# Kernel optimization log

Hardware: AMD Instinct MI355X
Metric: run time of the kernel (lower is better)

## Reference

```python
import jax, jax.numpy as jnp
import numpy as np

N = 50000
E = 800000
IN_DIM = 512
HID = 64
OUT = 64
HEADS = 4
NEG_SLOPE = 0.2


def setup_inputs() -> dict:
    key = jax.random.key(0)
    ks = jax.random.split(key, 16)
    s = 0.05
    inp = {
        "x": jax.random.normal(ks[0], (N, IN_DIM), jnp.float32),
        "edge_index": jax.random.randint(ks[1], (2, E), 0, N, jnp.int64),
        # layer 1: in=512 -> heads*hid = 4*64 = 256, concat=True
        "W1l": jax.random.normal(ks[2], (IN_DIM, HEADS * HID), jnp.float32) * s,
        "b1l": jnp.zeros((HEADS * HID,), jnp.float32),
        "W1r": jax.random.normal(ks[3], (IN_DIM, HEADS * HID), jnp.float32) * s,
        "b1r": jnp.zeros((HEADS * HID,), jnp.float32),
        "att1": jax.random.normal(ks[4], (HEADS, HID), jnp.float32) * s,
        "bias1": jnp.zeros((HEADS * HID,), jnp.float32),
        # layer 2: in=256 -> heads*(2*out) = 4*128, concat=False (mean heads)
        "W2l": jax.random.normal(ks[5], (HEADS * HID, HEADS * 2 * OUT), jnp.float32) * s,
        "b2l": jnp.zeros((HEADS * 2 * OUT,), jnp.float32),
        "W2r": jax.random.normal(ks[6], (HEADS * HID, HEADS * 2 * OUT), jnp.float32) * s,
        "b2r": jnp.zeros((HEADS * 2 * OUT,), jnp.float32),
        "att2": jax.random.normal(ks[7], (HEADS, 2 * OUT), jnp.float32) * s,
        "bias2": jnp.zeros((2 * OUT,), jnp.float32),
    }
    return inp


def _gatv2(x, src, dst, Wl, bl, Wr, br, att, bias, concat):
    """GATv2Conv (PyG semantics): message x_l[src], attention over incoming edges per dst."""
    H, C = att.shape
    n = x.shape[0]
    xl = (x @ Wl + bl).reshape(n, H, C)  # source transform (messages)
    xr = (x @ Wr + br).reshape(n, H, C)  # target transform
    g = jax.nn.leaky_relu(xl[src] + xr[dst], NEG_SLOPE)   # [E, H, C]
    e = jnp.einsum('ehc,hc->eh', g, att)                  # [E, H]
    # numerically-stable softmax over irregular neighbor sets (segmented by dst)
    m = jax.ops.segment_max(e, dst, num_segments=n)
    ex = jnp.exp(e - m[dst])
    denom = jax.ops.segment_sum(ex, dst, num_segments=n)
    alpha = ex / (denom[dst] + 1e-16)                     # [E, H]
    out = jax.ops.segment_sum(xl[src] * alpha[..., None], dst, num_segments=n)  # [N, H, C]
    if concat:
        return out.reshape(n, H * C) + bias
    return out.mean(axis=1) + bias


def reference(x, edge_index, W1l, b1l, W1r, b1r, att1, bias1,
              W2l, b2l, W2r, b2r, att2, bias2):
    # add self loops (PyG add_self_loops=True default)
    loops = jnp.arange(N, dtype=edge_index.dtype)
    src = jnp.concatenate([edge_index[0], loops])
    dst = jnp.concatenate([edge_index[1], loops])
    h = jax.nn.relu(_gatv2(x, src, dst, W1l, b1l, W1r, b1r, att1, bias1, concat=True))
    return _gatv2(h, src, dst, W2l, b2l, W2r, b2r, att2, bias2, concat=False)
```

## Files before the change

### kernel.cpp

```cpp
#include <hip/hip_runtime.h>

#define NNODES 50000
#define NEDGES 800000
#define ET (NEDGES + NNODES)
#define HEADS 4

typedef __attribute__((ext_vector_type(8))) short bf16x8;
typedef __attribute__((ext_vector_type(4))) float f32x4;
typedef __attribute__((ext_vector_type(2))) float f32x2v;

#define EXP2F(x) __builtin_amdgcn_exp2f(x)

#if defined(__has_builtin)
#if __has_builtin(__builtin_elementwise_fma)
#define VFMA(a, b, c) __builtin_elementwise_fma((a), (b), (c))
#endif
#if __has_builtin(__builtin_elementwise_max)
#define VMAX(a, b) __builtin_elementwise_max((a), (b))
#endif
#endif
#ifndef VFMA
__device__ inline f32x2v vfma_(f32x2v a, f32x2v b, f32x2v c) {
  f32x2v r; r.x = fmaf(a.x, b.x, c.x); r.y = fmaf(a.y, b.y, c.y); return r;
}
#define VFMA vfma_
#endif
#ifndef VMAX
__device__ inline f32x2v vmax_(f32x2v a, f32x2v b) {
  f32x2v r; r.x = fmaxf(a.x, b.x); r.y = fmaxf(a.y, b.y); return r;
}
#define VMAX vmax_
#endif

#define GLOAD16(g, l) __builtin_amdgcn_global_load_lds(                      \
    (const __attribute__((address_space(1))) unsigned int*)(g),              \
    (__attribute__((address_space(3))) unsigned int*)(l), 16, 0, 0)

__device__ inline unsigned short f2bf(float f) {
  union { float f; unsigned int i; } c; c.f = f;
  unsigned int b = c.i + 0x7fffu + ((c.i >> 16) & 1u);
  return (unsigned short)(b >> 16);
}
__device__ inline f32x2v cvtpair(unsigned u) {
  union { unsigned i; float f; } lo, hi;
  lo.i = u << 16; hi.i = u & 0xffff0000u;
  f32x2v r; r.x = lo.f; r.y = hi.f; return r;
}


__global__ void k_hist(const int* __restrict__ ei, int* __restrict__ deg) {
  int i = blockIdx.x * blockDim.x + threadIdx.x;
  if (i >= ET) return;
  int dst = (i < NEDGES) ? ei[NEDGES + i] : (i - NEDGES);
  atomicAdd(&deg[dst], 1);
}

__global__ void k_scan1(const int* __restrict__ deg, int* __restrict__ part,
                        int* __restrict__ bsum, int n) {
  __shared__ int s[256];
  int tid = threadIdx.x;
  int i = blockIdx.x * 256 + tid;
  int v = (i < n) ? deg[i] : 0;
  s[tid] = v;
  __syncthreads();
  for (int off = 1; off < 256; off <<= 1) {
    int t = (tid >= off) ? s[tid - off] : 0;
    __syncthreads();
    s[tid] += t;
    __syncthreads();
  }
  if (i < n) part[i] = s[tid] - v;
  if (tid == 255) bsum[blockIdx.x] = s[255];
}

__global__ void k_scan2(int* bsum, int nb) {
  __shared__ int s[256];
  int t = threadIdx.x;
  int v = (t < nb) ? bsum[t] : 0;
  s[t] = v;
  __syncthreads();
  for (int off = 1; off < 256; off <<= 1) {
    int tv = (t >= off) ? s[t - off] : 0;
    __syncthreads();
    s[t] += tv;
    __syncthreads();
  }
  if (t < nb) bsum[t] = s[t] - v;
}

__global__ void k_scan3(const int* __restrict__ part, const int* __restrict__ bsum,
                        int* __restrict__ rowstart, int* __restrict__ cursor,
                        int n, int total) {
  int i = blockIdx.x * blockDim.x + threadIdx.x;
  if (i < n) {
    int v = part[i] + bsum[i >> 8];
    rowstart[i] = v;
    cursor[i] = v;
  }
  if (i == n) rowstart[n] = total;
}

__global__ void k_scatter(const int* __restrict__ ei, int* __restrict__ cursor,
                          int* __restrict__ csrsrc) {
  int i = blockIdx.x * blockDim.x + threadIdx.x;
  if (i >= ET) return;
  int src, dst;
  if (i < NEDGES) { src = ei[i]; dst = ei[NEDGES + i]; }
  else            { src = dst = i - NEDGES; }
  int pos = atomicAdd(&cursor[dst], 1);
  csrsrc[pos] = src;
}


__global__ void k_cast_bf16(const float* __restrict__ in, unsigned short* __restrict__ out, int n4) {
  int i = blockIdx.x * blockDim.x + threadIdx.x;
  if (i >= n4) return;
  float4 v = ((const float4*)in)[i];
  ushort4 o;
  o.x = f2bf(v.x); o.y = f2bf(v.y); o.z = f2bf(v.z); o.w = f2bf(v.w);
  ((ushort4*)out)[i] = o;
}

__global__ __launch_bounds__(256) void k_castw_all(
    const float* __restrict__ W1l, const float* __restrict__ W1r,
    const float* __restrict__ W2l, const float* __restrict__ W2r,
    unsigned short* __restrict__ w1t, unsigned short* __restrict__ w2t) {
  __shared__ float tile[32][33];
  int which = blockIdx.y;
  const float* W;
  unsigned short* T;
  int K, N, noff;
  if (which == 0)      { W = W1l; T = w1t; K = 512; N = 256; noff = 0; }
  else if (which == 1) { W = W1r; T = w1t; K = 512; N = 256; noff = 256; }
  else if (which == 2) { W = W2l; T = w2t; K = 256; N = 512; noff = 0; }
  else                 { W = W2r; T = w2t; K = 256; N = 512; noff = 512; }
  int tpr = N >> 5;
  int tk = (blockIdx.x / tpr) << 5;
  int tn = (blockIdx.x % tpr) << 5;
  int c = threadIdx.x & 31, r = threadIdx.x >> 5;
#pragma unroll
  for (int rr = 0; rr < 32; rr += 8)
    tile[r + rr][c] = W[(size_t)(tk + r + rr) * N + tn + c];
  __syncthreads();
#pragma unroll
  for (int rr = 0; rr < 32; rr += 8)
    T[(size_t)(tn + r + rr + noff) * K + tk + c] = f2bf(tile[c][r + rr]);
}


template <int N> __device__ __forceinline__ void waitvm() {
  if constexpr (N == 0) asm volatile("s_waitcnt vmcnt(0)" ::: "memory");
  else if constexpr (N == 4) asm volatile("s_waitcnt vmcnt(4)" ::: "memory");
  else asm volatile("s_waitcnt vmcnt(8)" ::: "memory");
}

__global__ __launch_bounds__(256) void k_gemm(
    const unsigned short* __restrict__ A, const unsigned short* __restrict__ Bt,
    const float* __restrict__ bL, const float* __restrict__ bR, int nsplit,
    unsigned short* __restrict__ C, int M, int K, int N) {
  __shared__ unsigned short As[3][128 * 32];
  __shared__ unsigned short Bs[3][128 * 32];
  int tid = threadIdx.x;
  int lane = tid & 63, wave = tid >> 6;
  int wr = (wave >> 1) * 64, wc = (wave & 1) * 64;
  int row0 = blockIdx.x * 128, col0 = blockIdx.y * 128;
  int fr = lane & 15, fq = lane >> 4;
  int sr = tid >> 2, sc = (tid & 3) * 8;

  const unsigned short* ga0 = &A[(size_t)(row0 + sr) * K + sc];
  const unsigned short* ga1 = &A[(size_t)(row0 + sr + 64) * K + sc];
  const unsigned short* gb0 = &Bt[(size_t)(col0 + sr) * K + sc];
  const unsigned short* gb1 = &Bt[(size_t)(col0 + sr + 64) * K + sc];

  f32x4 acc[4][4] = {};
  const int NT = K >> 5;

#define STAGE(b, k0)                                  \
  do {                                                \
    GLOAD16(ga0 + (k0), &As[b][tid * 8]);             \
    GLOAD16(ga1 + (k0), &As[b][2048 + tid * 8]);      \
    GLOAD16(gb0 + (k0), &Bs[b][tid * 8]);             \
    GLOAD16(gb1 + (k0), &Bs[b][2048 + tid * 8]);      \
  } while (0)

#define COMPUTE(b)                                                        \
  do {                                                                    \
    bf16x8 af[4], bfr[4];                                                 \
    _Pragma("unroll")                                                     \
    for (int m = 0; m < 4; ++m)                                           \
      af[m] = *(const bf16x8*)&As[b][(wr + m * 16 + fr) * 32 + fq * 8];   \
    _Pragma("unroll")                                                     \
    for (int n = 0; n < 4; ++n)                                           \
      bfr[n] = *(const bf16x8*)&Bs[b][(wc + n * 16 + fr) * 32 + fq * 8];  \
    _Pragma("unroll")                                                     \
    for (int m = 0; m < 4; ++m)                                           \
      _Pragma("unroll")                                                   \
      for (int n = 0; n < 4; ++n)                                         \
        acc[m][n] = __builtin_amdgcn_mfma_f32_16x16x32_bf16(af[m], bfr[n], acc[m][n], 0, 0, 0); \
  } while (0)

  STAGE(0, 0);
  STAGE(1, 32);
  STAGE(2, 64);

  for (int t = 0; t < NT - 3; ++t) {
    int b = t % 3;
    waitvm<8>();
    __builtin_amdgcn_s_barrier();
    COMPUTE(b);
    asm volatile("s_waitcnt lgkmcnt(0)" ::: "memory");
    __builtin_amdgcn_sched_barrier(0);
    __builtin_amdgcn_s_barrier();
    STAGE(b, (t + 3) << 5);
  }
  waitvm<8>(); __builtin_amdgcn_s_barrier(); COMPUTE((NT - 3) % 3);
  waitvm<4>(); __builtin_amdgcn_s_barrier(); COMPUTE((NT - 2) % 3);
  waitvm<0>(); __builtin_amdgcn_s_barrier(); COMPUTE((NT - 1) % 3);

#undef STAGE
#undef COMPUTE

#pragma unroll
  for (int m = 0; m < 4; ++m) {
#pragma unroll
    for (int n = 0; n < 4; ++n) {
      int col = col0 + wc + n * 16 + fr;
      float bv = (col < nsplit) ? bL[col] : bR[col - nsplit];
#pragma unroll
      for (int j = 0; j < 4; ++j) {
        int row = row0 + wr + m * 16 + fq * 4 + j;
        if (row < M) C[(size_t)row * N + col] = f2bf(acc[m][n][j] + bv);
      }
    }
  }
}


template <int CQ> struct raw_t;
template <> struct raw_t<1> { using T = uint2; };
template <> struct raw_t<2> { using T = uint4; };

template <int CQ>
__device__ __forceinline__ void rawwords(const typename raw_t<CQ>::T& r, unsigned* u) {
  u[0] = r.x; u[1] = r.y;
  if constexpr (CQ == 2) { u[2] = r.z; u[3] = r.w; }
}

template <int CQ>
__device__ __forceinline__ void unpackP(const typename raw_t<CQ>::T& r, f32x2v* x) {
  unsigned u[4];
  rawwords<CQ>(r, u);
#pragma unroll
  for (int j = 0; j < CQ * 2; ++j) x[j] = cvtpair(u[j]);
}

template <int CQ>
__device__ __forceinline__ float edge_score_pk(const f32x2v* x, const f32x2v* xr2,
                                               const f32x2v* att2) {
  const f32x2v c02 = {0.2f, 0.2f};
  f32x2v p2 = {0.f, 0.f};
#pragma unroll
  for (int j = 0; j < CQ * 2; ++j) {
    f32x2v s = x[j] + xr2[j];
    f32x2v g = VMAX(s, s * c02);
    p2 = VFMA(att2[j], g, p2);
  }
  return p2.x + p2.y;
}

template <int CQ, int MODE, int STR>
__global__ __launch_bounds__(256) void k_fused(
    const int* __restrict__ rowstart, const int* __restrict__ csrsrc,
    const unsigned short* __restrict__ xlr,
    const float* __restrict__ att, const float* __restrict__ bias,
    void* __restrict__ outp) {
  const int C = CQ * 64;
  const int CHL = CQ * 4;
  const int P = CQ * 2;
  using RawT = typename raw_t<CQ>::T;
  int dst = (blockIdx.x * blockDim.x + threadIdx.x) >> 6;
  int lane = threadIdx.x & 63;
  if (dst >= NNODES) return;
  int h = lane >> 4;
  int l = lane & 15;
  const int choff = h * C + l * CHL;

  f32x2v xr2[P], att2[P];
  {
    RawT xrr = *(const RawT*)&xlr[(size_t)dst * STR + STR / 2 + choff];
    unpackP<CQ>(xrr, xr2);
#pragma unroll
    for (int j = 0; j < P; ++j) {
      att2[j].x = att[choff + j * 2 + 0] * 1.44269504f;
      att2[j].y = att[choff + j * 2 + 1] * 1.44269504f;
    }
  }

  int rs = __builtin_amdgcn_readfirstlane(rowstart[dst]);
  int re = __builtin_amdgcn_readfirstlane(rowstart[dst + 1]);

  float den = 0.f;
  f32x2v acc2[P];
#pragma unroll
  for (int j = 0; j < P; ++j) acc2[j] = (f32x2v){0.f, 0.f};

  int i = rs;
  for (; i + 4 <= re; i += 4) {
    int s0 = csrsrc[i + 0];
    int s1 = csrsrc[i + 1];
    int s2 = csrsrc[i + 2];
    int s3 = csrsrc[i + 3];
    RawT r0 = *(const RawT*)&xlr[(unsigned)s0 * (unsigned)STR + choff];
    RawT r1 = *(const RawT*)&xlr[(unsigned)s1 * (unsigned)STR + choff];
    RawT r2 = *(const RawT*)&xlr[(unsigned)s2 * (unsigned)STR + choff];
    RawT r3 = *(const RawT*)&xlr[(unsigned)s3 * (unsigned)STR + choff];
    f32x2v x0[P], x1[P], x2[P], x3[P];
    unpackP<CQ>(r0, x0); unpackP<CQ>(r1, x1);
    unpackP<CQ>(r2, x2); unpackP<CQ>(r3, x3);
    float p0 = edge_score_pk<CQ>(x0, xr2, att2);
    float p1 = edge_score_pk<CQ>(x1, xr2, att2);
    float p2 = edge_score_pk<CQ>(x2, xr2, att2);
    float p3 = edge_score_pk<CQ>(x3, xr2, att2);
#pragma unroll
    for (int d = 1; d <= 8; d <<= 1) {
      p0 += __shfl_xor(p0, d);
      p1 += __shfl_xor(p1, d);
      p2 += __shfl_xor(p2, d);
      p3 += __shfl_xor(p3, d);
    }
    float w0 = EXP2F(p0), w1 = EXP2F(p1), w2 = EXP2F(p2), w3 = EXP2F(p3);
    den += (w0 + w1) + (w2 + w3);
    f32x2v w0v = {w0, w0}, w1v = {w1, w1}, w2v = {w2, w2}, w3v = {w3, w3};
#pragma unroll
    for (int j = 0; j < P; ++j) {
      f32x2v a = acc2[j];
      a = VFMA(w0v, x0[j], a);
      a = VFMA(w1v, x1[j], a);
      a = VFMA(w2v, x2[j], a);
      a = VFMA(w3v, x3[j], a);
      acc2[j] = a;
    }
  }
  for (; i < re; ++i) {
    int s0 = csrsrc[i];
    RawT r0 = *(const RawT*)&xlr[(unsigned)s0 * (unsigned)STR + choff];
    f32x2v x0[P];
    unpackP<CQ>(r0, x0);
    float p0 = edge_score_pk<CQ>(x0, xr2, att2);
#pragma unroll
    for (int d = 1; d <= 8; d <<= 1) p0 += __shfl_xor(p0, d);
    float w0 = EXP2F(p0);
    den += w0;
    f32x2v wv = {w0, w0};
#pragma unroll
    for (int j = 0; j < P; ++j) acc2[j] = VFMA(wv, x0[j], acc2[j]);
  }

  float inv = 1.f / (den + 1e-16f);

  if (MODE == 0) {
    unsigned short* out = (unsigned short*)outp;
#pragma unroll
    for (int q = 0; q < CQ; ++q) {
      const float4 bv = *(const float4*)&bias[choff + q * 4];
      ushort4 o;
      o.x = f2bf(fmaxf(acc2[q * 2 + 0].x * inv + bv.x, 0.f));
      o.y = f2bf(fmaxf(acc2[q * 2 + 0].y * inv + bv.y, 0.f));
      o.z = f2bf(fmaxf(acc2[q * 2 + 1].x * inv + bv.z, 0.f));
      o.w = f2bf(fmaxf(acc2[q * 2 + 1].y * inv + bv.w, 0.f));
      *(ushort4*)&out[(size_t)dst * (HEADS * C) + choff + q * 4] = o;
    }
  } else {
    float* out = (float*)outp;
    float rr[8];
#pragma unroll
    for (int j = 0; j < P; ++j) {
      rr[j * 2 + 0] = acc2[j].x * inv;
      rr[j * 2 + 1] = acc2[j].y * inv;
    }
#pragma unroll
    for (int c = 0; c < CHL; ++c) {
      rr[c] += __shfl_xor(rr[c], 16);
      rr[c] += __shfl_xor(rr[c], 32);
    }
    if (lane < 16) {
#pragma unroll
      for (int q = 0; q < CQ; ++q) {
        int c = lane * CHL + q * 4;
        float4 o;
        o.x = rr[q * 4 + 0] * 0.25f + bias[c + 0];
        o.y = rr[q * 4 + 1] * 0.25f + bias[c + 1];
        o.z = rr[q * 4 + 2] * 0.25f + bias[c + 2];
        o.w = rr[q * 4 + 3] * 0.25f + bias[c + 3];
        *(float4*)&out[(size_t)dst * C + c] = o;
      }
    }
  }
}


extern "C" void kernel_launch(void* const* d_in, const int* in_sizes, int n_in,
                              void* d_out, int out_size, void* d_ws, size_t ws_size,
                              hipStream_t stream) {
  (void)in_sizes; (void)n_in; (void)out_size; (void)ws_size;
  const float* x     = (const float*)d_in[0];
  const int*   ei    = (const int*)d_in[1];
  const float* W1l   = (const float*)d_in[2];
  const float* b1l   = (const float*)d_in[3];
  const float* W1r   = (const float*)d_in[4];
  const float* b1r   = (const float*)d_in[5];
  const float* att1  = (const float*)d_in[6];
  const float* bias1 = (const float*)d_in[7];
  const float* W2l   = (const float*)d_in[8];
  const float* b2l   = (const float*)d_in[9];
  const float* W2r   = (const float*)d_in[10];
  const float* b2r   = (const float*)d_in[11];
  const float* att2  = (const float*)d_in[12];
  const float* bias2 = (const float*)d_in[13];
  float* out = (float*)d_out;

  char* ws = (char*)d_ws;
  size_t off = 0;
  auto alloc = [&](size_t bytes) {
    char* p = ws + off;
    off = (off + bytes + 255) & ~(size_t)255;
    return p;
  };
  int*  deg      = (int*)alloc((size_t)NNODES * 4);
  int*  part     = (int*)alloc((size_t)NNODES * 4);
  int*  bsum     = (int*)alloc(256 * 4);
  int*  rowstart = (int*)alloc((size_t)(NNODES + 1) * 4);
  int*  cursor   = (int*)alloc((size_t)NNODES * 4);
  int*  csrsrc   = (int*)alloc((size_t)ET * 4);
  unsigned short* xb   = (unsigned short*)alloc((size_t)NNODES * 512 * 2);
  unsigned short* w1t  = (unsigned short*)alloc((size_t)512 * 512 * 2);
  unsigned short* w2t  = (unsigned short*)alloc((size_t)1024 * 256 * 2);
  unsigned short* xlr1 = (unsigned short*)alloc((size_t)NNODES * 512 * 2);
  unsigned short* hbuf = (unsigned short*)alloc((size_t)NNODES * 256 * 2);
  unsigned short* xlr2 = (unsigned short*)alloc((size_t)NNODES * 1024 * 2);
  (void)alloc(64 * 1024);

  (void)hipMemsetAsync(deg, 0, (size_t)NNODES * 4, stream);
  k_hist<<<(ET + 255) / 256, 256, 0, stream>>>(ei, deg);
  int nb = (NNODES + 255) / 256;
  k_scan1<<<nb, 256, 0, stream>>>(deg, part, bsum, NNODES);
  k_scan2<<<1, 256, 0, stream>>>(bsum, nb);
  k_scan3<<<(NNODES + 256) / 256, 256, 0, stream>>>(part, bsum, rowstart, cursor, NNODES, ET);
  k_scatter<<<(ET + 255) / 256, 256, 0, stream>>>(ei, cursor, csrsrc);

  k_cast_bf16<<<(NNODES * 512 / 4 + 255) / 256, 256, 0, stream>>>(x, xb, NNODES * 512 / 4);
  k_castw_all<<<dim3(128, 4), 256, 0, stream>>>(W1l, W1r, W2l, W2r, w1t, w2t);

  const int gridM = (NNODES + 127) / 128;
  const int gridFused = (NNODES + 3) / 4;

  k_gemm<<<dim3(gridM, 4), 256, 0, stream>>>(xb, w1t, b1l, b1r, 256, xlr1, NNODES, 512, 512);
  k_fused<1, 0, 512><<<gridFused, 256, 0, stream>>>(rowstart, csrsrc, xlr1, att1, bias1, hbuf);

  k_gemm<<<dim3(gridM, 8), 256, 0, stream>>>(hbuf, w2t, b2l, b2r, 512, xlr2, NNODES, 256, 1024);
  k_fused<2, 1, 1024><<<gridFused, 256, 0, stream>>>(rowstart, csrsrc, xlr2, att2, bias2, out);
}
```

Before: 448.0 us.

## Pipeline layer-2 neighbor gathers through LDS and merge prep kernels

Layer-2 aggregation now prefetches source-node feature rows into a per-wave LDS slab with global_load_lds, keeping eight gathers in flight at once. Edges are processed in masked batches of eight so load latency overlaps with compute. The x cast, degree histogram and weight transpose are merged into one launch to cut launch count. The CSR index buffer gains padding so the masked prefetch can read past the end safely, at the cost of wasted gathers on the padded slots of low-degree nodes.

```diff
diff --git a/kernel.cpp b/kernel.cpp
--- a/kernel.cpp
+++ b/kernel.cpp
@@ -46,14 +46,65 @@
   lo.i = u << 16; hi.i = u & 0xffff0000u;
   f32x2v r; r.x = lo.f; r.y = hi.f; return r;
 }
-
-
-__global__ void k_hist(const int* __restrict__ ei, int* __restrict__ deg) {
-  int i = blockIdx.x * blockDim.x + threadIdx.x;
-  if (i >= ET) return;
-  int dst = (i < NEDGES) ? ei[NEDGES + i] : (i - NEDGES);
-  atomicAdd(&deg[dst], 1);
-}
+__device__ inline float4 b4tof(uint2 r) {
+  float4 f;
+  union { unsigned int i; float v; } c;
+  c.i = r.x << 16;          f.x = c.v;
+  c.i = r.x & 0xffff0000u;  f.y = c.v;
+  c.i = r.y << 16;          f.z = c.v;
+  c.i = r.y & 0xffff0000u;  f.w = c.v;
+  return f;
+}
+
+
+#define CASTB 25000
+#define HISTB ((ET + 255) / 256)
+#define PREPB (CASTB + HISTB + 512)
+
+__global__ __launch_bounds__(256) void k_prep(
+    const int* __restrict__ ei, int* __restrict__ deg,
+    const float* __restrict__ x, unsigned short* __restrict__ xb,
+    const float* __restrict__ W1l, const float* __restrict__ W1r,
+    const float* __restrict__ W2l, const float* __restrict__ W2r,
+    unsigned short* __restrict__ w1t, unsigned short* __restrict__ w2t) {
+  __shared__ float tile[32][33];
+  int b = blockIdx.x;
+  if (b < CASTB) {
+    int i = b * 256 + threadIdx.x;
+    float4 v = ((const float4*)x)[i];
+    ushort4 o;
+    o.x = f2bf(v.x); o.y = f2bf(v.y); o.z = f2bf(v.z); o.w = f2bf(v.w);
+    ((ushort4*)xb)[i] = o;
+  } else if (b < CASTB + HISTB) {
+    int i = (b - CASTB) * 256 + threadIdx.x;
+    if (i < ET) {
+      int dst = (i < NEDGES) ? ei[NEDGES + i] : (i - NEDGES);
+      atomicAdd(&deg[dst], 1);
+    }
+  } else {
+    int bb = b - CASTB - HISTB;
+    int which = bb >> 7, bx = bb & 127;
+    const float* W;
+    unsigned short* T;
+    int K, N, noff;
+    if (which == 0)      { W = W1l; T = w1t; K = 512; N = 256; noff = 0; }
+    else if (which == 1) { W = W1r; T = w1t; K = 512; N = 256; noff = 256; }
+    else if (which == 2) { W = W2l; T = w2t; K = 256; N = 512; noff = 0; }
+    else                 { W = W2r; T = w2t; K = 256; N = 512; noff = 512; }
+    int tpr = N >> 5;
+    int tk = (bx / tpr) << 5;
+    int tn = (bx % tpr) << 5;
+    int c = threadIdx.x & 31, r = threadIdx.x >> 5;
+#pragma unroll
+    for (int rr = 0; rr < 32; rr += 8)
+      tile[r + rr][c] = W[(size_t)(tk + r + rr) * N + tn + c];
+    __syncthreads();
+#pragma unroll
+    for (int rr = 0; rr < 32; rr += 8)
+      T[(size_t)(tn + r + rr + noff) * K + tk + c] = f2bf(tile[c][r + rr]);
+  }
+}
+
 
 __global__ void k_scan1(const int* __restrict__ deg, int* __restrict__ part,
                         int* __restrict__ bsum, int n) {
@@ -109,42 +160,6 @@
   else            { src = dst = i - NEDGES; }
   int pos = atomicAdd(&cursor[dst], 1);
   csrsrc[pos] = src;
-}
-
-
-__global__ void k_cast_bf16(const float* __restrict__ in, unsigned short* __restrict__ out, int n4) {
-  int i = blockIdx.x * blockDim.x + threadIdx.x;
-  if (i >= n4) return;
-  float4 v = ((const float4*)in)[i];
-  ushort4 o;
-  o.x = f2bf(v.x); o.y = f2bf(v.y); o.z = f2bf(v.z); o.w = f2bf(v.w);
-  ((ushort4*)out)[i] = o;
-}
-
-__global__ __launch_bounds__(256) void k_castw_all(
-    const float* __restrict__ W1l, const float* __restrict__ W1r,
-    const float* __restrict__ W2l, const float* __restrict__ W2r,
-    unsigned short* __restrict__ w1t, unsigned short* __restrict__ w2t) {
-  __shared__ float tile[32][33];
-  int which = blockIdx.y;
-  const float* W;
-  unsigned short* T;
-  int K, N, noff;
-  if (which == 0)      { W = W1l; T = w1t; K = 512; N = 256; noff = 0; }
-  else if (which == 1) { W = W1r; T = w1t; K = 512; N = 256; noff = 256; }
-  else if (which == 2) { W = W2l; T = w2t; K = 256; N = 512; noff = 0; }
-  else                 { W = W2r; T = w2t; K = 256; N = 512; noff = 512; }
-  int tpr = N >> 5;
-  int tk = (blockIdx.x / tpr) << 5;
-  int tn = (blockIdx.x % tpr) << 5;
-  int c = threadIdx.x & 31, r = threadIdx.x >> 5;
-#pragma unroll
-  for (int rr = 0; rr < 32; rr += 8)
-    tile[r + rr][c] = W[(size_t)(tk + r + rr) * N + tn + c];
-  __syncthreads();
-#pragma unroll
-  for (int rr = 0; rr < 32; rr += 8)
-    T[(size_t)(tn + r + rr + noff) * K + tk + c] = f2bf(tile[c][r + rr]);
 }
 
 
@@ -240,87 +255,58 @@
 template <> struct raw_t<1> { using T = uint2; };
 template <> struct raw_t<2> { using T = uint4; };
 
-template <int CQ>
-__device__ __forceinline__ void rawwords(const typename raw_t<CQ>::T& r, unsigned* u) {
-  u[0] = r.x; u[1] = r.y;
-  if constexpr (CQ == 2) { u[2] = r.z; u[3] = r.w; }
-}
-
-template <int CQ>
-__device__ __forceinline__ void unpackP(const typename raw_t<CQ>::T& r, f32x2v* x) {
-  unsigned u[4];
-  rawwords<CQ>(r, u);
-#pragma unroll
-  for (int j = 0; j < CQ * 2; ++j) x[j] = cvtpair(u[j]);
-}
-
-template <int CQ>
-__device__ __forceinline__ float edge_score_pk(const f32x2v* x, const f32x2v* xr2,
-                                               const f32x2v* att2) {
-  const f32x2v c02 = {0.2f, 0.2f};
-  f32x2v p2 = {0.f, 0.f};
-#pragma unroll
-  for (int j = 0; j < CQ * 2; ++j) {
-    f32x2v s = x[j] + xr2[j];
-    f32x2v g = VMAX(s, s * c02);
-    p2 = VFMA(att2[j], g, p2);
-  }
-  return p2.x + p2.y;
-}
-
-template <int CQ, int MODE, int STR>
-__global__ __launch_bounds__(256) void k_fused(
+__global__ __launch_bounds__(256) void k_fused1(
     const int* __restrict__ rowstart, const int* __restrict__ csrsrc,
     const unsigned short* __restrict__ xlr,
     const float* __restrict__ att, const float* __restrict__ bias,
-    void* __restrict__ outp) {
-  const int C = CQ * 64;
-  const int CHL = CQ * 4;
-  const int P = CQ * 2;
-  using RawT = typename raw_t<CQ>::T;
+    unsigned short* __restrict__ out) {
+  const int STR = 512, C = 64;
   int dst = (blockIdx.x * blockDim.x + threadIdx.x) >> 6;
   int lane = threadIdx.x & 63;
   if (dst >= NNODES) return;
-  int h = lane >> 4;
-  int l = lane & 15;
-  const int choff = h * C + l * CHL;
-
-  f32x2v xr2[P], att2[P];
+  int h = lane >> 4, l = lane & 15;
+  const int choff = h * C + l * 4;
+
+  f32x2v xr2[2], att2[2];
   {
-    RawT xrr = *(const RawT*)&xlr[(size_t)dst * STR + STR / 2 + choff];
-    unpackP<CQ>(xrr, xr2);
-#pragma unroll
-    for (int j = 0; j < P; ++j) {
+    uint2 xrr = *(const uint2*)&xlr[(size_t)dst * STR + 256 + choff];
+    xr2[0] = cvtpair(xrr.x); xr2[1] = cvtpair(xrr.y);
+#pragma unroll
+    for (int j = 0; j < 2; ++j) {
       att2[j].x = att[choff + j * 2 + 0] * 1.44269504f;
       att2[j].y = att[choff + j * 2 + 1] * 1.44269504f;
     }
   }
+  const f32x2v c02 = {0.2f, 0.2f};
 
   int rs = __builtin_amdgcn_readfirstlane(rowstart[dst]);
   int re = __builtin_amdgcn_readfirstlane(rowstart[dst + 1]);
 
   float den = 0.f;
-  f32x2v acc2[P];
-#pragma unroll
-  for (int j = 0; j < P; ++j) acc2[j] = (f32x2v){0.f, 0.f};
+  f32x2v acc2[2] = {{0.f, 0.f}, {0.f, 0.f}};
 
   int i = rs;
   for (; i + 4 <= re; i += 4) {
-    int s0 = csrsrc[i + 0];
-    int s1 = csrsrc[i + 1];
-    int s2 = csrsrc[i + 2];
-    int s3 = csrsrc[i + 3];
-    RawT r0 = *(const RawT*)&xlr[(unsigned)s0 * (unsigned)STR + choff];
-    RawT r1 = *(const RawT*)&xlr[(unsigned)s1 * (unsigned)STR + choff];
-    RawT r2 = *(const RawT*)&xlr[(unsigned)s2 * (unsigned)STR + choff];
-    RawT r3 = *(const RawT*)&xlr[(unsigned)s3 * (unsigned)STR + choff];
-    f32x2v x0[P], x1[P], x2[P], x3[P];
-    unpackP<CQ>(r0, x0); unpackP<CQ>(r1, x1);
-    unpackP<CQ>(r2, x2); unpackP<CQ>(r3, x3);
-    float p0 = edge_score_pk<CQ>(x0, xr2, att2);
-    float p1 = edge_score_pk<CQ>(x1, xr2, att2);
-    float p2 = edge_score_pk<CQ>(x2, xr2, att2);
-    float p3 = edge_score_pk<CQ>(x3, xr2, att2);
+    int s0 = csrsrc[i + 0], s1 = csrsrc[i + 1];
+    int s2 = csrsrc[i + 2], s3 = csrsrc[i + 3];
+    uint2 r0 = *(const uint2*)&xlr[(unsigned)s0 * (unsigned)STR + choff];
+    uint2 r1 = *(const uint2*)&xlr[(unsigned)s1 * (unsigned)STR + choff];
+    uint2 r2 = *(const uint2*)&xlr[(unsigned)s2 * (unsigned)STR + choff];
+    uint2 r3 = *(const uint2*)&xlr[(unsigned)s3 * (unsigned)STR + choff];
+    f32x2v x0[2] = {cvtpair(r0.x), cvtpair(r0.y)};
+    f32x2v x1[2] = {cvtpair(r1.x), cvtpair(r1.y)};
+    f32x2v x2[2] = {cvtpair(r2.x), cvtpair(r2.y)};
+    f32x2v x3[2] = {cvtpair(r3.x), cvtpair(r3.y)};
+    f32x2v q0 = {0.f, 0.f}, q1 = {0.f, 0.f}, q2 = {0.f, 0.f}, q3 = {0.f, 0.f};
+#pragma unroll
+    for (int j = 0; j < 2; ++j) {
+      f32x2v s;
+      s = x0[j] + xr2[j]; q0 = VFMA(att2[j], VMAX(s, s * c02), q0);
+      s = x1[j] + xr2[j]; q1 = VFMA(att2[j], VMAX(s, s * c02), q1);
+      s = x2[j] + xr2[j]; q2 = VFMA(att2[j], VMAX(s, s * c02), q2);
+      s = x3[j] + xr2[j]; q3 = VFMA(att2[j], VMAX(s, s * c02), q3);
+    }
+    float p0 = q0.x + q0.y, p1 = q1.x + q1.y, p2 = q2.x + q2.y, p3 = q3.x + q3.y;
 #pragma unroll
     for (int d = 1; d <= 8; d <<= 1) {
       p0 += __shfl_xor(p0, d);
@@ -332,7 +318,7 @@
     den += (w0 + w1) + (w2 + w3);
     f32x2v w0v = {w0, w0}, w1v = {w1, w1}, w2v = {w2, w2}, w3v = {w3, w3};
 #pragma unroll
-    for (int j = 0; j < P; ++j) {
+    for (int j = 0; j < 2; ++j) {
       f32x2v a = acc2[j];
       a = VFMA(w0v, x0[j], a);
       a = VFMA(w1v, x1[j], a);
@@ -343,57 +329,137 @@
   }
   for (; i < re; ++i) {
     int s0 = csrsrc[i];
-    RawT r0 = *(const RawT*)&xlr[(unsigned)s0 * (unsigned)STR + choff];
-    f32x2v x0[P];
-    unpackP<CQ>(r0, x0);
-    float p0 = edge_score_pk<CQ>(x0, xr2, att2);
+    uint2 r0 = *(const uint2*)&xlr[(unsigned)s0 * (unsigned)STR + choff];
+    f32x2v x0[2] = {cvtpair(r0.x), cvtpair(r0.y)};
+    f32x2v q0 = {0.f, 0.f};
+#pragma unroll
+    for (int j = 0; j < 2; ++j) {
+      f32x2v s = x0[j] + xr2[j];
+      q0 = VFMA(att2[j], VMAX(s, s * c02), q0);
+    }
+    float p0 = q0.x + q0.y;
 #pragma unroll
     for (int d = 1; d <= 8; d <<= 1) p0 += __shfl_xor(p0, d);
     float w0 = EXP2F(p0);
     den += w0;
     f32x2v wv = {w0, w0};
 #pragma unroll
-    for (int j = 0; j < P; ++j) acc2[j] = VFMA(wv, x0[j], acc2[j]);
+    for (int j = 0; j < 2; ++j) acc2[j] = VFMA(wv, x0[j], acc2[j]);
   }
 
   float inv = 1.f / (den + 1e-16f);
-
-  if (MODE == 0) {
-    unsigned short* out = (unsigned short*)outp;
-#pragma unroll
-    for (int q = 0; q < CQ; ++q) {
-      const float4 bv = *(const float4*)&bias[choff + q * 4];
-      ushort4 o;
-      o.x = f2bf(fmaxf(acc2[q * 2 + 0].x * inv + bv.x, 0.f));
-      o.y = f2bf(fmaxf(acc2[q * 2 + 0].y * inv + bv.y, 0.f));
-      o.z = f2bf(fmaxf(acc2[q * 2 + 1].x * inv + bv.z, 0.f));
-      o.w = f2bf(fmaxf(acc2[q * 2 + 1].y * inv + bv.w, 0.f));
-      *(ushort4*)&out[(size_t)dst * (HEADS * C) + choff + q * 4] = o;
-    }
-  } else {
-    float* out = (float*)outp;
-    float rr[8];
-#pragma unroll
-    for (int j = 0; j < P; ++j) {
-      rr[j * 2 + 0] = acc2[j].x * inv;
-      rr[j * 2 + 1] = acc2[j].y * inv;
-    }
-#pragma unroll
-    for (int c = 0; c < CHL; ++c) {
-      rr[c] += __shfl_xor(rr[c], 16);
-      rr[c] += __shfl_xor(rr[c], 32);
-    }
-    if (lane < 16) {
-#pragma unroll
-      for (int q = 0; q < CQ; ++q) {
-        int c = lane * CHL + q * 4;
-        float4 o;
-        o.x = rr[q * 4 + 0] * 0.25f + bias[c + 0];
-        o.y = rr[q * 4 + 1] * 0.25f + bias[c + 1];
-        o.z = rr[q * 4 + 2] * 0.25f + bias[c + 2];
-        o.w = rr[q * 4 + 3] * 0.25f + bias[c + 3];
-        *(float4*)&out[(size_t)dst * C + c] = o;
+  const float4 bv = *(const float4*)&bias[choff];
+  ushort4 o;
+  o.x = f2bf(fmaxf(acc2[0].x * inv + bv.x, 0.f));
+  o.y = f2bf(fmaxf(acc2[0].y * inv + bv.y, 0.f));
+  o.z = f2bf(fmaxf(acc2[1].x * inv + bv.z, 0.f));
+  o.w = f2bf(fmaxf(acc2[1].y * inv + bv.w, 0.f));
+  *(ushort4*)&out[(size_t)dst * 256 + choff] = o;
+}
+
+
+__global__ __launch_bounds__(256) void k_fused2(
+    const int* __restrict__ rowstart, const int* __restrict__ csrsrc,
+    const unsigned short* __restrict__ xlr,
+    const float* __restrict__ att, const float* __restrict__ bias,
+    float* __restrict__ out) {
+  __shared__ char slab_[4][8 * 1024];
+  int dst = (blockIdx.x * blockDim.x + threadIdx.x) >> 6;
+  int lane = threadIdx.x & 63;
+  if (dst >= NNODES) return;
+  char* slab = slab_[threadIdx.x >> 6];
+  int h = lane >> 4, l = lane & 15;
+  const int choff = h * 128 + l * 8;
+
+  f32x2v xr2[4], att2[4];
+  {
+    uint4 xrr = *(const uint4*)&xlr[(size_t)dst * 1024 + 512 + choff];
+    unsigned u[4] = {xrr.x, xrr.y, xrr.z, xrr.w};
+#pragma unroll
+    for (int j = 0; j < 4; ++j) {
+      xr2[j] = cvtpair(u[j]);
+      att2[j].x = att[choff + j * 2 + 0] * 1.44269504f;
+      att2[j].y = att[choff + j * 2 + 1] * 1.44269504f;
+    }
+  }
+  const f32x2v c02 = {0.2f, 0.2f};
+
+  int rs = __builtin_amdgcn_readfirstlane(rowstart[dst]);
+  int re = __builtin_amdgcn_readfirstlane(rowstart[dst + 1]);
+  int nb = (re - rs + 7) >> 3;
+
+  float den = 0.f;
+  f32x2v acc2[4] = {{0.f, 0.f}, {0.f, 0.f}, {0.f, 0.f}, {0.f, 0.f}};
+
+  int idxN[8];
+#pragma unroll
+  for (int e = 0; e < 8; ++e) {
+    int v = csrsrc[rs + e];
+    v = (rs + e < re) ? v : 0;
+    GLOAD16(&xlr[(unsigned)v * 1024u + choff], slab + e * 1024 + lane * 16);
+  }
+#pragma unroll
+  for (int e = 0; e < 8; ++e) idxN[e] = csrsrc[rs + 8 + e];
+
+  int i = rs;
+  for (int b = 0; b < nb; ++b, i += 8) {
+#pragma unroll
+    for (int e = 0; e < 8; ++e) {
+      asm volatile("s_waitcnt vmcnt(7)" ::: "memory");
+      uint4 raw = *(const uint4*)(slab + e * 1024 + lane * 16);
+      asm volatile("s_waitcnt lgkmcnt(0)" ::: "memory");
+      {
+        int v = (i + 8 + e < re) ? idxN[e] : 0;
+        GLOAD16(&xlr[(unsigned)v * 1024u + choff], slab + e * 1024 + lane * 16);
+        idxN[e] = csrsrc[i + 16 + e];
       }
+      unsigned u[4] = {raw.x, raw.y, raw.z, raw.w};
+      f32x2v x[4];
+#pragma unroll
+      for (int j = 0; j < 4; ++j) x[j] = cvtpair(u[j]);
+      f32x2v p2 = {0.f, 0.f};
+#pragma unroll
+      for (int j = 0; j < 4; ++j) {
+        f32x2v s = x[j] + xr2[j];
+        p2 = VFMA(att2[j], VMAX(s, s * c02), p2);
+      }
+      float p = p2.x + p2.y;
+      p += __shfl_xor(p, 1);
+      p += __shfl_xor(p, 2);
+      p += __shfl_xor(p, 4);
+      p += __shfl_xor(p, 8);
+      p = (i + e < re) ? p : -1e30f;
+      float w = EXP2F(p);
+      den += w;
+      f32x2v wv = {w, w};
+#pragma unroll
+      for (int j = 0; j < 4; ++j) acc2[j] = VFMA(wv, x[j], acc2[j]);
+    }
+  }
+  asm volatile("s_waitcnt vmcnt(0)" ::: "memory");
+
+  float inv = 1.f / (den + 1e-16f);
+  float rr[8];
+#pragma unroll
+  for (int j = 0; j < 4; ++j) {
+    rr[j * 2 + 0] = acc2[j].x * inv;
+    rr[j * 2 + 1] = acc2[j].y * inv;
+  }
+#pragma unroll
+  for (int c = 0; c < 8; ++c) {
+    rr[c] += __shfl_xor(rr[c], 16);
+    rr[c] += __shfl_xor(rr[c], 32);
+  }
+  if (lane < 16) {
+#pragma unroll
+    for (int q = 0; q < 2; ++q) {
+      int c = lane * 8 + q * 4;
+      float4 o;
+      o.x = rr[q * 4 + 0] * 0.25f + bias[c + 0];
+      o.y = rr[q * 4 + 1] * 0.25f + bias[c + 1];
+      o.z = rr[q * 4 + 2] * 0.25f + bias[c + 2];
+      o.w = rr[q * 4 + 3] * 0.25f + bias[c + 3];
+      *(float4*)&out[(size_t)dst * 128 + c] = o;
     }
   }
 }
@@ -431,7 +497,7 @@
   int*  bsum     = (int*)alloc(256 * 4);
   int*  rowstart = (int*)alloc((size_t)(NNODES + 1) * 4);
   int*  cursor   = (int*)alloc((size_t)NNODES * 4);
-  int*  csrsrc   = (int*)alloc((size_t)ET * 4);
+  int*  csrsrc   = (int*)alloc((size_t)(ET + 32) * 4);
   unsigned short* xb   = (unsigned short*)alloc((size_t)NNODES * 512 * 2);
   unsigned short* w1t  = (unsigned short*)alloc((size_t)512 * 512 * 2);
   unsigned short* w2t  = (unsigned short*)alloc((size_t)1024 * 256 * 2);
@@ -441,22 +507,21 @@
   (void)alloc(64 * 1024);
 
   (void)hipMemsetAsync(deg, 0, (size_t)NNODES * 4, stream);
-  k_hist<<<(ET + 255) / 256, 256, 0, stream>>>(ei, deg);
+
+  k_prep<<<PREPB, 256, 0, stream>>>(ei, deg, x, xb, W1l, W1r, W2l, W2r, w1t, w2t);
+
   int nb = (NNODES + 255) / 256;
   k_scan1<<<nb, 256, 0, stream>>>(deg, part, bsum, NNODES);
   k_scan2<<<1, 256, 0, stream>>>(bsum, nb);
   k_scan3<<<(NNODES + 256) / 256, 256, 0, stream>>>(part, bsum, rowstart, cursor, NNODES, ET);
   k_scatter<<<(ET + 255) / 256, 256, 0, stream>>>(ei, cursor, csrsrc);
 
-  k_cast_bf16<<<(NNODES * 512 / 4 + 255) / 256, 256, 0, stream>>>(x, xb, NNODES * 512 / 4);
-  k_castw_all<<<dim3(128, 4), 256, 0, stream>>>(W1l, W1r, W2l, W2r, w1t, w2t);
-
   const int gridM = (NNODES + 127) / 128;
   const int gridFused = (NNODES + 3) / 4;
 
   k_gemm<<<dim3(gridM, 4), 256, 0, stream>>>(xb, w1t, b1l, b1r, 256, xlr1, NNODES, 512, 512);
-  k_fused<1, 0, 512><<<gridFused, 256, 0, stream>>>(rowstart, csrsrc, xlr1, att1, bias1, hbuf);
+  k_fused1<<<gridFused, 256, 0, stream>>>(rowstart, csrsrc, xlr1, att1, bias1, hbuf);
 
   k_gemm<<<dim3(gridM, 8), 256, 0, stream>>>(hbuf, w2t, b2l, b2r, 512, xlr2, NNODES, 256, 1024);
-  k_fused<2, 1, 1024><<<gridFused, 256, 0, stream>>>(rowstart, csrsrc, xlr2, att2, bias2, out);
-}
+  k_fused2<<<gridFused, 256, 0, stream>>>(rowstart, csrsrc, xlr2, att2, bias2, out);
+}
```

Result: slower. 496.9 us (+10.9%).

## Merge prep kernels and process destination nodes in degree-sorted order

Applied to the files above, without the earlier changes.

Fuses the x cast, degree histogram and weight transpose-cast into one launch to cut kernel launch count. Adds a counting sort of nodes by in-degree (bin, scan, scatter) and has the fused aggregation kernels map waves to nodes through this permutation. Waves in the same block then see similar edge counts, which reduces load imbalance and tail effects. In exchange it adds three small kernels plus an extra indirection, and it gives up the locality of processing consecutive destination nodes.

```diff
diff --git a/kernel.cpp b/kernel.cpp
--- a/kernel.cpp
+++ b/kernel.cpp
@@ -48,12 +48,54 @@
 }
 
 
-__global__ void k_hist(const int* __restrict__ ei, int* __restrict__ deg) {
-  int i = blockIdx.x * blockDim.x + threadIdx.x;
-  if (i >= ET) return;
-  int dst = (i < NEDGES) ? ei[NEDGES + i] : (i - NEDGES);
-  atomicAdd(&deg[dst], 1);
-}
+#define CASTB 25000
+#define HISTB ((ET + 255) / 256)
+#define PREPB (CASTB + HISTB + 512)
+
+__global__ __launch_bounds__(256) void k_prep(
+    const int* __restrict__ ei, int* __restrict__ deg,
+    const float* __restrict__ x, unsigned short* __restrict__ xb,
+    const float* __restrict__ W1l, const float* __restrict__ W1r,
+    const float* __restrict__ W2l, const float* __restrict__ W2r,
+    unsigned short* __restrict__ w1t, unsigned short* __restrict__ w2t) {
+  __shared__ float tile[32][33];
+  int b = blockIdx.x;
+  if (b < CASTB) {
+    int i = b * 256 + threadIdx.x;
+    float4 v = ((const float4*)x)[i];
+    ushort4 o;
+    o.x = f2bf(v.x); o.y = f2bf(v.y); o.z = f2bf(v.z); o.w = f2bf(v.w);
+    ((ushort4*)xb)[i] = o;
+  } else if (b < CASTB + HISTB) {
+    int i = (b - CASTB) * 256 + threadIdx.x;
+    if (i < ET) {
+      int dst = (i < NEDGES) ? ei[NEDGES + i] : (i - NEDGES);
+      atomicAdd(&deg[dst], 1);
+    }
+  } else {
+    int bb = b - CASTB - HISTB;
+    int which = bb >> 7, bx = bb & 127;
+    const float* W;
+    unsigned short* T;
+    int K, N, noff;
+    if (which == 0)      { W = W1l; T = w1t; K = 512; N = 256; noff = 0; }
+    else if (which == 1) { W = W1r; T = w1t; K = 512; N = 256; noff = 256; }
+    else if (which == 2) { W = W2l; T = w2t; K = 256; N = 512; noff = 0; }
+    else                 { W = W2r; T = w2t; K = 256; N = 512; noff = 512; }
+    int tpr = N >> 5;
+    int tk = (bx / tpr) << 5;
+    int tn = (bx % tpr) << 5;
+    int c = threadIdx.x & 31, r = threadIdx.x >> 5;
+#pragma unroll
+    for (int rr = 0; rr < 32; rr += 8)
+      tile[r + rr][c] = W[(size_t)(tk + r + rr) * N + tn + c];
+    __syncthreads();
+#pragma unroll
+    for (int rr = 0; rr < 32; rr += 8)
+      T[(size_t)(tn + r + rr + noff) * K + tk + c] = f2bf(tile[c][r + rr]);
+  }
+}
+
 
 __global__ void k_scan1(const int* __restrict__ deg, int* __restrict__ part,
                         int* __restrict__ bsum, int n) {
@@ -112,39 +154,40 @@
 }
 
 
-__global__ void k_cast_bf16(const float* __restrict__ in, unsigned short* __restrict__ out, int n4) {
+__global__ void k_dbin(const int* __restrict__ deg, int* __restrict__ dbin) {
   int i = blockIdx.x * blockDim.x + threadIdx.x;
-  if (i >= n4) return;
-  float4 v = ((const float4*)in)[i];
-  ushort4 o;
-  o.x = f2bf(v.x); o.y = f2bf(v.y); o.z = f2bf(v.z); o.w = f2bf(v.w);
-  ((ushort4*)out)[i] = o;
-}
-
-__global__ __launch_bounds__(256) void k_castw_all(
-    const float* __restrict__ W1l, const float* __restrict__ W1r,
-    const float* __restrict__ W2l, const float* __restrict__ W2r,
-    unsigned short* __restrict__ w1t, unsigned short* __restrict__ w2t) {
-  __shared__ float tile[32][33];
-  int which = blockIdx.y;
-  const float* W;
-  unsigned short* T;
-  int K, N, noff;
-  if (which == 0)      { W = W1l; T = w1t; K = 512; N = 256; noff = 0; }
-  else if (which == 1) { W = W1r; T = w1t; K = 512; N = 256; noff = 256; }
-  else if (which == 2) { W = W2l; T = w2t; K = 256; N = 512; noff = 0; }
-  else                 { W = W2r; T = w2t; K = 256; N = 512; noff = 512; }
-  int tpr = N >> 5;
-  int tk = (blockIdx.x / tpr) << 5;
-  int tn = (blockIdx.x % tpr) << 5;
-  int c = threadIdx.x & 31, r = threadIdx.x >> 5;
-#pragma unroll
-  for (int rr = 0; rr < 32; rr += 8)
-    tile[r + rr][c] = W[(size_t)(tk + r + rr) * N + tn + c];
+  if (i < NNODES) atomicAdd(&dbin[min(deg[i], 1023)], 1);
+}
+
+__global__ void k_dscan(int* __restrict__ dbin) {
+  __shared__ int s[1024];
+  int t = threadIdx.x;
+  int o[4];
+#pragma unroll
+  for (int k = 0; k < 4; ++k) { o[k] = dbin[t * 4 + k]; s[t * 4 + k] = o[k]; }
   __syncthreads();
-#pragma unroll
-  for (int rr = 0; rr < 32; rr += 8)
-    T[(size_t)(tn + r + rr + noff) * K + tk + c] = f2bf(tile[c][r + rr]);
+  for (int off = 1; off < 1024; off <<= 1) {
+    int v[4];
+#pragma unroll
+    for (int k = 0; k < 4; ++k) {
+      int j = t * 4 + k;
+      v[k] = (j >= off) ? s[j - off] : 0;
+    }
+    __syncthreads();
+#pragma unroll
+    for (int k = 0; k < 4; ++k) s[t * 4 + k] += v[k];
+    __syncthreads();
+  }
+#pragma unroll
+  for (int k = 0; k < 4; ++k) dbin[t * 4 + k] = s[t * 4 + k] - o[k];
+}
+
+__global__ void k_dscat(const int* __restrict__ deg, int* __restrict__ dbin,
+                        int* __restrict__ perm) {
+  int i = blockIdx.x * blockDim.x + threadIdx.x;
+  if (i >= NNODES) return;
+  int pos = atomicAdd(&dbin[min(deg[i], 1023)], 1);
+  perm[pos] = i;
 }
 
 
@@ -241,17 +284,9 @@
 template <> struct raw_t<2> { using T = uint4; };
 
 template <int CQ>
-__device__ __forceinline__ void rawwords(const typename raw_t<CQ>::T& r, unsigned* u) {
-  u[0] = r.x; u[1] = r.y;
-  if constexpr (CQ == 2) { u[2] = r.z; u[3] = r.w; }
-}
-
-template <int CQ>
 __device__ __forceinline__ void unpackP(const typename raw_t<CQ>::T& r, f32x2v* x) {
-  unsigned u[4];
-  rawwords<CQ>(r, u);
-#pragma unroll
-  for (int j = 0; j < CQ * 2; ++j) x[j] = cvtpair(u[j]);
+  x[0] = cvtpair(r.x); x[1] = cvtpair(r.y);
+  if constexpr (CQ == 2) { x[2] = cvtpair(r.z); x[3] = cvtpair(r.w); }
 }
 
 template <int CQ>
@@ -271,6 +306,7 @@
 template <int CQ, int MODE, int STR>
 __global__ __launch_bounds__(256) void k_fused(
     const int* __restrict__ rowstart, const int* __restrict__ csrsrc,
+    const int* __restrict__ perm,
     const unsigned short* __restrict__ xlr,
     const float* __restrict__ att, const float* __restrict__ bias,
     void* __restrict__ outp) {
@@ -278,9 +314,10 @@
   const int CHL = CQ * 4;
   const int P = CQ * 2;
   using RawT = typename raw_t<CQ>::T;
-  int dst = (blockIdx.x * blockDim.x + threadIdx.x) >> 6;
+  int wid = (blockIdx.x * blockDim.x + threadIdx.x) >> 6;
   int lane = threadIdx.x & 63;
-  if (dst >= NNODES) return;
+  if (wid >= NNODES) return;
+  int dst = __builtin_amdgcn_readfirstlane(perm[wid]);
   int h = lane >> 4;
   int l = lane & 15;
   const int choff = h * C + l * CHL;
@@ -431,7 +468,9 @@
   int*  bsum     = (int*)alloc(256 * 4);
   int*  rowstart = (int*)alloc((size_t)(NNODES + 1) * 4);
   int*  cursor   = (int*)alloc((size_t)NNODES * 4);
-  int*  csrsrc   = (int*)alloc((size_t)ET * 4);
+  int*  csrsrc   = (int*)alloc((size_t)(ET + 32) * 4);
+  int*  dbin     = (int*)alloc(1024 * 4);
+  int*  perm     = (int*)alloc((size_t)NNODES * 4);
   unsigned short* xb   = (unsigned short*)alloc((size_t)NNODES * 512 * 2);
   unsigned short* w1t  = (unsigned short*)alloc((size_t)512 * 512 * 2);
   unsigned short* w2t  = (unsigned short*)alloc((size_t)1024 * 256 * 2);
@@ -441,22 +480,25 @@
   (void)alloc(64 * 1024);
 
   (void)hipMemsetAsync(deg, 0, (size_t)NNODES * 4, stream);
-  k_hist<<<(ET + 255) / 256, 256, 0, stream>>>(ei, deg);
+  (void)hipMemsetAsync(dbin, 0, 1024 * 4, stream);
+
+  k_prep<<<PREPB, 256, 0, stream>>>(ei, deg, x, xb, W1l, W1r, W2l, W2r, w1t, w2t);
+
   int nb = (NNODES + 255) / 256;
   k_scan1<<<nb, 256, 0, stream>>>(deg, part, bsum, NNODES);
+  k_dbin<<<nb, 256, 0, stream>>>(deg, dbin);
   k_scan2<<<1, 256, 0, stream>>>(bsum, nb);
+  k_dscan<<<1, 256, 0, stream>>>(dbin);
   k_scan3<<<(NNODES + 256) / 256, 256, 0, stream>>>(part, bsum, rowstart, cursor, NNODES, ET);
+  k_dscat<<<nb, 256, 0, stream>>>(deg, dbin, perm);
   k_scatter<<<(ET + 255) / 256, 256, 0, stream>>>(ei, cursor, csrsrc);
-
-  k_cast_bf16<<<(NNODES * 512 / 4 + 255) / 256, 256, 0, stream>>>(x, xb, NNODES * 512 / 4);
-  k_castw_all<<<dim3(128, 4), 256, 0, stream>>>(W1l, W1r, W2l, W2r, w1t, w2t);
 
   const int gridM = (NNODES + 127) / 128;
   const int gridFused = (NNODES + 3) / 4;
 
   k_gemm<<<dim3(gridM, 4), 256, 0, stream>>>(xb, w1t, b1l, b1r, 256, xlr1, NNODES, 512, 512);
-  k_fused<1, 0, 512><<<gridFused, 256, 0, stream>>>(rowstart, csrsrc, xlr1, att1, bias1, hbuf);
+  k_fused<1, 0, 512><<<gridFused, 256, 0, stream>>>(rowstart, csrsrc, perm, xlr1, att1, bias1, hbuf);
 
   k_gemm<<<dim3(gridM, 8), 256, 0, stream>>>(hbuf, w2t, b2l, b2r, 512, xlr2, NNODES, 256, 1024);
-  k_fused<2, 1, 1024><<<gridFused, 256, 0, stream>>>(rowstart, csrsrc, xlr2, att2, bias2, out);
-}
+  k_fused<2, 1, 1024><<<gridFused, 256, 0, stream>>>(rowstart, csrsrc, perm, xlr2, att2, bias2, out);
+}
```

Result: slower. 733.0 us (+63.6%).
